# Kernel tuning notes

Measured on AMD Instinct MI355X. Metric: run time of the kernel, lower is better.

Reference implementation:

```python
import jax, jax.numpy as jnp
import numpy as np
from jax import lax

STRIDE = 2
PADDING = 2
EPS = 1e-5


def _conv1d(x, w):
    # x: (N, C_in, T), w: (C_out, C_in, K) -> (N, C_out, T_out)
    return lax.conv_general_dilated(
        x, w, window_strides=(STRIDE,), padding=[(PADDING, PADDING)],
        dimension_numbers=("NCH", "OIH", "NCH"))


def setup_inputs() -> dict:
    key = jax.random.key(0)
    ks = jax.random.split(key, 5)
    Batch, num_sensors, in_c, out_c, k, T, r = 32, 8, 64, 128, 5, 2048, 8
    x = jax.random.normal(ks[0], (Batch * num_sensors, in_c, T), dtype=jnp.float32)
    A_flat = jax.random.normal(ks[1], (Batch, r * in_c * k), dtype=jnp.float32) * 0.02
    B_flat = jax.random.normal(ks[2], (Batch, out_c * r), dtype=jnp.float32) * 0.02
    fan_in = in_c * k
    conv_w = jax.random.normal(ks[3], (out_c, in_c, k), dtype=jnp.float32) / np.sqrt(fan_in)
    conv_b = jax.random.normal(ks[4], (out_c,), dtype=jnp.float32) * 0.01
    gamma = jnp.ones((out_c,), dtype=jnp.float32)
    beta = jnp.zeros((out_c,), dtype=jnp.float32)
    return {"x": x, "A_flat": A_flat, "B_flat": B_flat,
            "conv_w": conv_w, "conv_b": conv_b, "gamma": gamma, "beta": beta,
            "num_sensors": num_sensors, "r": r, "lora_scale": 0.5}


def reference(x, A_flat, B_flat, conv_w, conv_b, gamma, beta, num_sensors, r, lora_scale):
    Batch = A_flat.shape[0]
    out_c, in_c, k = conv_w.shape
    T = x.shape[-1]

    # base conv1d
    out_base = _conv1d(x, conv_w) + conv_b[None, :, None]  # (B*S, out_c, T_out)

    # dynamic per-sample LoRA delta weight: delta_W = B @ A, (Batch, out_c, in_c, k)
    A = A_flat.reshape(Batch, r, in_c * k)
    B_mat = B_flat.reshape(Batch, out_c, r)
    delta_W = jnp.einsum("bor,brm->bom", B_mat, A).reshape(Batch, out_c, in_c, k)
    delta_W = delta_W * lora_scale

    # per-sample conv: sensors of one sample share that sample's delta weight
    x_b = x.reshape(Batch, num_sensors, in_c, T)
    lora_out = jax.vmap(_conv1d)(x_b, delta_W)  # (Batch, S, out_c, T_out)
    lora_out = lora_out.reshape(Batch * num_sensors, out_c, -1)

    out = jax.nn.relu(out_base + lora_out)

    # GroupNorm, num_groups = min(4, out_c) reduced until divisible
    G = min(4, out_c)
    while out_c % G != 0:
        G -= 1
    N, C, To = out.shape
    og = out.reshape(N, G, C // G, To)
    mean = og.mean(axis=(2, 3), keepdims=True)
    var = og.var(axis=(2, 3), keepdims=True)
    normed = ((og - mean) * lax.rsqrt(var + EPS)).reshape(N, C, To)
    return normed * gamma[None, :, None] + beta[None, :, None]
```

## Files before the change

kernel.cpp:

```cpp
#include <hip/hip_runtime.h>
#include <hip/hip_bf16.h>

#define EPSV 1e-5f
#define PITCH 36
#define TILE_SH (66 * PITCH)
#define WTILE_SH (2 * TILE_SH)

typedef short bf16x8 __attribute__((ext_vector_type(8)));
typedef short bf16x4 __attribute__((ext_vector_type(4)));
typedef float f32x4  __attribute__((ext_vector_type(4)));

__device__ __forceinline__ short f2bf(float f){
  unsigned u = __float_as_uint(f);
  u += 0x7fff + ((u >> 16) & 1);
  return (short)(u >> 16);
}
__device__ __forceinline__ int pk2(float a, float b){
  __hip_bfloat162 h = __float22bfloat162_rn(float2{a, b});
  return *reinterpret_cast<int*>(&h);
}

__global__ void build_weights(const float* __restrict__ A_flat,
                              const float* __restrict__ B_flat,
                              const float* __restrict__ conv_w,
                              const float* __restrict__ scale_p,
                              short* __restrict__ Wb){
  int idx = blockIdx.x * 256 + threadIdx.x;
  int ci = idx & 63;
  int co = (idx >> 6) & 127;
  int bj = idx >> 13;
  int b  = bj / 5;
  int j  = bj - 5 * b;
  int m  = ci * 5 + j;
  const float* Bp = B_flat + (b * 128 + co) * 8;
  const float* Ap = A_flat + b * 8 * 320 + m;
  float d = 0.f;
#pragma unroll
  for (int r = 0; r < 8; ++r) d = fmaf(Bp[r], Ap[r * 320], d);
  float w = conv_w[co * 320 + m] + scale_p[0] * d;
  Wb[idx] = f2bf(w);
}

__global__ __launch_bounds__(512, 4)
void conv_gn_mfma(const float* __restrict__ x,
                  const short* __restrict__ Wb,
                  const float* __restrict__ conv_b,
                  const float* __restrict__ gamma,
                  const float* __restrict__ beta,
                  float* __restrict__ out){
  __shared__ short xt[8 * WTILE_SH];
  __shared__ float redS[8], redQ[8], bc2[2];

  const int bid    = blockIdx.x;
  const int sample = ((bid & 7) << 5) + (bid >> 5);
  const int g      = (bid >> 3) & 3;
  const int b      = sample >> 3;
  const int tid    = threadIdx.x;
  const int lane   = tid & 63;
  const int wid    = tid >> 6;
  const int l16    = lane & 15;
  const int lk     = lane >> 4;

  short* xe = xt + wid * WTILE_SH;
  short* xo = xe + TILE_SH;

  f32x4 acc[2][8];
#pragma unroll
  for (int m2 = 0; m2 < 2; ++m2)
#pragma unroll
    for (int n = 0; n < 8; ++n) acc[m2][n] = (f32x4){0.f,0.f,0.f,0.f};

  const size_t wb_base = (size_t)b * 5 * 128 * 64;
  const float* xsamp = x + (size_t)sample * 64 * 2048;

#pragma unroll
  for (int ph = 0; ph < 4; ++ph) {
    const int ch = ph >> 1;
    const int th = ph & 1;
    const int T0 = th * 512 + wid * 64;

    const float* xb = xsamp + (size_t)(ch * 32) * 2048;

    {
      const int c = 2 * T0 + 2 * (int)lane;
#pragma unroll
      for (int rg = 0; rg < 8; ++rg) {
        const float* r = xb + (size_t)(rg * 4) * 2048 + c;
        float2 v0 = *(const float2*)(r);
        float2 v1 = *(const float2*)(r + 2048);
        float2 v2 = *(const float2*)(r + 4096);
        float2 v3 = *(const float2*)(r + 6144);
        int2 ev = { pk2(v0.x, v1.x), pk2(v2.x, v3.x) };
        int2 od = { pk2(v0.y, v1.y), pk2(v2.y, v3.y) };
        *(int2*)(xe + (lane + 1) * PITCH + rg * 4) = ev;
        *(int2*)(xo + (lane + 1) * PITCH + rg * 4) = od;
      }
      if (lane < 32) {
        const int ci = lane;
        float2 h{0.f, 0.f};
        if (T0 > 0) h = *(const float2*)(xb + (size_t)ci * 2048 + (2 * T0 - 2));
        xe[ci] = f2bf(h.x);
        xo[ci] = f2bf(h.y);
      } else {
        const int ci = lane - 32;
        const int xc = 2 * T0 + 128;
        float v = (xc < 2048) ? xb[(size_t)ci * 2048 + xc] : 0.f;
        xe[65 * PITCH + ci] = f2bf(v);
      }
    }

#pragma unroll
    for (int j = 0; j < 5; ++j) {
      const short* apb = Wb + wb_base + (size_t)(j * 128 + g * 32) * 64 + ch * 32 + lk * 8;
      bf16x8 a0 = *(const bf16x8*)(apb + (size_t)l16 * 64);
      bf16x8 a1 = *(const bf16x8*)(apb + (size_t)(l16 + 16) * 64);
      const short* arr = (j & 1) ? xo : xe;
      const int joff = (j & 1) ? ((j - 1) >> 1) : (j >> 1);
#pragma unroll
      for (int nn = 0; nn < 4; ++nn) {
        int tl = nn * 16 + l16;
        const short* bp = arr + (tl + joff) * PITCH + lk * 8;
        bf16x4 lo = *(const bf16x4*)bp;
        bf16x4 hi = *(const bf16x4*)(bp + 4);
        bf16x8 bfr = {lo[0],lo[1],lo[2],lo[3],hi[0],hi[1],hi[2],hi[3]};
        const int n = th * 4 + nn;
        acc[0][n] = __builtin_amdgcn_mfma_f32_16x16x32_bf16(a0, bfr, acc[0][n], 0, 0, 0);
        acc[1][n] = __builtin_amdgcn_mfma_f32_16x16x32_bf16(a1, bfr, acc[1][n], 0, 0, 0);
      }
    }
  }

  float cb_[2][4], ga_[2][4], be_[2][4];
#pragma unroll
  for (int m2 = 0; m2 < 2; ++m2)
#pragma unroll
    for (int r = 0; r < 4; ++r) {
      int co = g * 32 + m2 * 16 + lk * 4 + r;
      cb_[m2][r] = conv_b[co];
      ga_[m2][r] = gamma[co];
      be_[m2][r] = beta[co];
    }
  float s1 = 0.f, s2 = 0.f;
#pragma unroll
  for (int m2 = 0; m2 < 2; ++m2)
#pragma unroll
    for (int n = 0; n < 8; ++n)
#pragma unroll
      for (int r = 0; r < 4; ++r) {
        float v = acc[m2][n][r] + cb_[m2][r];
        v = v > 0.f ? v : 0.f;
        acc[m2][n][r] = v;
        s1 += v;
        s2 = fmaf(v, v, s2);
      }
#pragma unroll
  for (int off = 32; off; off >>= 1) {
    s1 += __shfl_down(s1, off);
    s2 += __shfl_down(s2, off);
  }
  if (lane == 0) { redS[wid] = s1; redQ[wid] = s2; }
  __syncthreads();
  if (tid == 0) {
    float a = 0.f, q = 0.f;
#pragma unroll
    for (int w = 0; w < 8; ++w) { a += redS[w]; q += redQ[w]; }
    float mean = a * (1.f / 32768.f);
    float var  = q * (1.f / 32768.f) - mean * mean;
    bc2[0] = mean;
    bc2[1] = rsqrtf(var + EPSV);
  }
  __syncthreads();
  const float mean = bc2[0], inv = bc2[1];
  float* ob = out + (size_t)sample * 128 * 1024;
#pragma unroll
  for (int m2 = 0; m2 < 2; ++m2)
#pragma unroll
    for (int r = 0; r < 4; ++r) {
      int co = g * 32 + m2 * 16 + lk * 4 + r;
      float aa = ga_[m2][r] * inv;
      float bb = be_[m2][r] - mean * aa;
      float* orow = ob + (size_t)co * 1024 + l16;
#pragma unroll
      for (int n = 0; n < 8; ++n) {
        int t = (n >> 2) * 512 + wid * 64 + (n & 3) * 16;
        orow[t] = acc[m2][n][r] * aa + bb;
      }
    }
}

extern "C" void kernel_launch(void* const* d_in, const int* in_sizes, int n_in,
                              void* d_out, int out_size, void* d_ws, size_t ws_size,
                              hipStream_t stream) {
  const float* x       = (const float*)d_in[0];
  const float* A_flat  = (const float*)d_in[1];
  const float* B_flat  = (const float*)d_in[2];
  const float* conv_w  = (const float*)d_in[3];
  const float* conv_b  = (const float*)d_in[4];
  const float* gamma   = (const float*)d_in[5];
  const float* beta    = (const float*)d_in[6];
  const float* scale_p = (const float*)d_in[9];

  float* out = (float*)d_out;
  short* Wb  = (short*)d_ws;

  build_weights<<<5120, 256, 0, stream>>>(A_flat, B_flat, conv_w, scale_p, Wb);
  conv_gn_mfma<<<1024, 512, 0, stream>>>(x, Wb, conv_b, gamma, beta, out);
}
```

Measured before the change: 111.5 us.

## Pre-transpose input to bf16 time-major layout and read MMA operands directly

Adds a separate transpose kernel that converts x to a padded bf16 (time, channel) layout in the workspace, so the conv kernel loads MFMA B fragments straight from global memory without per-block LDS staging. Each conv block previously rebuilt the converted tile four times (once per output-channel group), and this pass removes that repeated fp32 load and convert work. In exchange it adds a full extra read and write of a bf16 copy of x plus one more launch. It falls back to the old kernel when the workspace is too small.

```diff
diff --git a/kernel.cpp b/kernel.cpp
--- a/kernel.cpp
+++ b/kernel.cpp
@@ -2,9 +2,6 @@
 #include <hip/hip_bf16.h>
 
 #define EPSV 1e-5f
-#define PITCH 36
-#define TILE_SH (66 * PITCH)
-#define WTILE_SH (2 * TILE_SH)
 
 typedef short bf16x8 __attribute__((ext_vector_type(8)));
 typedef short bf16x4 __attribute__((ext_vector_type(4)));
@@ -41,14 +38,64 @@
   Wb[idx] = f2bf(w);
 }
 
+#define XP 66
+__global__ __launch_bounds__(256, 8)
+void xpose(const float* __restrict__ x, short* __restrict__ xT){
+  __shared__ short xl[512 * XP];
+  const int bid  = blockIdx.x;
+  const int s    = bid >> 2;
+  const int q    = bid & 3;
+  const int tid  = threadIdx.x;
+  const int lane = tid & 63;
+  const int wid  = tid >> 6;
+
+  const float* xs = x + (size_t)s * 64 * 2048 + q * 512;
+#pragma unroll
+  for (int grp = 0; grp < 4; ++grp) {
+    const int ci0 = wid * 16 + grp * 4;
+    const float* xr = xs + (size_t)ci0 * 2048;
+#pragma unroll
+    for (int pass = 0; pass < 2; ++pass) {
+      int c0 = pass * 256 + lane * 4;
+      float4 v0 = *(const float4*)(xr + c0);
+      float4 v1 = *(const float4*)(xr + c0 + 2048);
+      float4 v2 = *(const float4*)(xr + c0 + 4096);
+      float4 v3 = *(const float4*)(xr + c0 + 6144);
+      const float a0[4] = {v0.x, v0.y, v0.z, v0.w};
+      const float a1[4] = {v1.x, v1.y, v1.z, v1.w};
+      const float a2[4] = {v2.x, v2.y, v2.z, v2.w};
+      const float a3[4] = {v3.x, v3.y, v3.z, v3.w};
+#pragma unroll
+      for (int k = 0; k < 4; ++k) {
+        int base = (c0 + k) * XP + ci0;
+        *(int*)&xl[base]     = pk2(a0[k], a1[k]);
+        *(int*)&xl[base + 2] = pk2(a2[k], a3[k]);
+      }
+    }
+  }
+  __syncthreads();
+
+  short* dst = xT + ((size_t)s * 2052 + 2 + q * 512) * 64;
+  const int ci4 = lane & 15;
+#pragma unroll
+  for (int it = 0; it < 32; ++it) {
+    int col = wid * 128 + it * 4 + (lane >> 4);
+    int base = col * XP + ci4 * 4;
+    int r0 = *(const int*)&xl[base];
+    int r1 = *(const int*)&xl[base + 2];
+    *(int2*)(dst + (size_t)col * 64 + ci4 * 4) = int2{r0, r1};
+  }
+  if (q == 0 && tid < 64) ((int*)(xT + (size_t)s * 2052 * 64))[tid] = 0;
+  if (q == 3 && tid < 64) ((int*)(xT + ((size_t)s * 2052 + 2050) * 64))[tid] = 0;
+}
+
 __global__ __launch_bounds__(512, 4)
-void conv_gn_mfma(const float* __restrict__ x,
-                  const short* __restrict__ Wb,
-                  const float* __restrict__ conv_b,
-                  const float* __restrict__ gamma,
-                  const float* __restrict__ beta,
-                  float* __restrict__ out){
-  __shared__ short xt[8 * WTILE_SH];
+void conv_gn_direct(const short* __restrict__ xT,
+                    const short* __restrict__ Wb,
+                    const float* __restrict__ conv_b,
+                    const float* __restrict__ gamma,
+                    const float* __restrict__ beta,
+                    float* __restrict__ out){
   __shared__ float redS[8], redQ[8], bc2[2];
 
   const int bid    = blockIdx.x;
@@ -60,55 +107,148 @@
   const int wid    = tid >> 6;
   const int l16    = lane & 15;
   const int lk     = lane >> 4;
-
+  const int T0     = wid << 7;
+
+  f32x4 acc[2][8];
+#pragma unroll
+  for (int m2 = 0; m2 < 2; ++m2)
+#pragma unroll
+    for (int n = 0; n < 8; ++n) acc[m2][n] = (f32x4){0.f,0.f,0.f,0.f};
+
+  const size_t wb_base = (size_t)b * 5 * 128 * 64;
+
+#pragma unroll
+  for (int ch = 0; ch < 2; ++ch) {
+    const short* xbase = xT + ((size_t)sample * 2052 + 2 * (T0 + l16)) * 64
+                            + ch * 32 + lk * 8;
+#pragma unroll
+    for (int j = 0; j < 5; ++j) {
+      const short* apb = Wb + wb_base + (size_t)(j * 128 + g * 32) * 64 + ch * 32 + lk * 8;
+      bf16x8 a0 = *(const bf16x8*)(apb + (size_t)l16 * 64);
+      bf16x8 a1 = *(const bf16x8*)(apb + (size_t)(l16 + 16) * 64);
+#pragma unroll
+      for (int nn = 0; nn < 8; ++nn) {
+        bf16x8 bfr = *(const bf16x8*)(xbase + nn * 2048 + j * 64);
+        acc[0][nn] = __builtin_amdgcn_mfma_f32_16x16x32_bf16(a0, bfr, acc[0][nn], 0, 0, 0);
+        acc[1][nn] = __builtin_amdgcn_mfma_f32_16x16x32_bf16(a1, bfr, acc[1][nn], 0, 0, 0);
+      }
+    }
+  }
+
+  float cb_[2][4], ga_[2][4], be_[2][4];
+#pragma unroll
+  for (int m2 = 0; m2 < 2; ++m2)
+#pragma unroll
+    for (int r = 0; r < 4; ++r) {
+      int co = g * 32 + m2 * 16 + lk * 4 + r;
+      cb_[m2][r] = conv_b[co];
+      ga_[m2][r] = gamma[co];
+      be_[m2][r] = beta[co];
+    }
+  float s1 = 0.f, s2 = 0.f;
+#pragma unroll
+  for (int m2 = 0; m2 < 2; ++m2)
+#pragma unroll
+    for (int n = 0; n < 8; ++n)
+#pragma unroll
+      for (int r = 0; r < 4; ++r) {
+        float v = acc[m2][n][r] + cb_[m2][r];
+        v = v > 0.f ? v : 0.f;
+        acc[m2][n][r] = v;
+        s1 += v;
+        s2 = fmaf(v, v, s2);
+      }
+#pragma unroll
+  for (int off = 32; off; off >>= 1) {
+    s1 += __shfl_down(s1, off);
+    s2 += __shfl_down(s2, off);
+  }
+  if (lane == 0) { redS[wid] = s1; redQ[wid] = s2; }
+  __syncthreads();
+  if (tid == 0) {
+    float a = 0.f, q = 0.f;
+#pragma unroll
+    for (int w = 0; w < 8; ++w) { a += redS[w]; q += redQ[w]; }
+    float mean = a * (1.f / 32768.f);
+    float var  = q * (1.f / 32768.f) - mean * mean;
+    bc2[0] = mean;
+    bc2[1] = rsqrtf(var + EPSV);
+  }
+  __syncthreads();
+  const float mean = bc2[0], inv = bc2[1];
+  float* ob = out + (size_t)sample * 128 * 1024;
+#pragma unroll
+  for (int m2 = 0; m2 < 2; ++m2)
+#pragma unroll
+    for (int r = 0; r < 4; ++r) {
+      int co = g * 32 + m2 * 16 + lk * 4 + r;
+      float aa = ga_[m2][r] * inv;
+      float bb = be_[m2][r] - mean * aa;
+      float* orow = ob + (size_t)co * 1024 + T0 + l16;
+#pragma unroll
+      for (int n = 0; n < 8; ++n)
+        orow[n * 16] = acc[m2][n][r] * aa + bb;
+    }
+}
+
+#define PITCH 36
+#define TILE_SH (66 * PITCH)
+#define WTILE_SH (2 * TILE_SH)
+__global__ __launch_bounds__(512, 4)
+void conv_gn_fallback(const float* __restrict__ x,
+                      const short* __restrict__ Wb,
+                      const float* __restrict__ conv_b,
+                      const float* __restrict__ gamma,
+                      const float* __restrict__ beta,
+                      float* __restrict__ out){
+  __shared__ short xt[8 * WTILE_SH];
+  __shared__ float redS[8], redQ[8], bc2[2];
+  const int bid    = blockIdx.x;
+  const int sample = ((bid & 7) << 5) + (bid >> 5);
+  const int g      = (bid >> 3) & 3;
+  const int b      = sample >> 3;
+  const int tid    = threadIdx.x;
+  const int lane   = tid & 63;
+  const int wid    = tid >> 6;
+  const int l16    = lane & 15;
+  const int lk     = lane >> 4;
   short* xe = xt + wid * WTILE_SH;
   short* xo = xe + TILE_SH;
-
   f32x4 acc[2][8];
 #pragma unroll
   for (int m2 = 0; m2 < 2; ++m2)
 #pragma unroll
     for (int n = 0; n < 8; ++n) acc[m2][n] = (f32x4){0.f,0.f,0.f,0.f};
-
   const size_t wb_base = (size_t)b * 5 * 128 * 64;
   const float* xsamp = x + (size_t)sample * 64 * 2048;
-
 #pragma unroll
   for (int ph = 0; ph < 4; ++ph) {
-    const int ch = ph >> 1;
-    const int th = ph & 1;
+    const int ch = ph >> 1, th = ph & 1;
     const int T0 = th * 512 + wid * 64;
-
     const float* xb = xsamp + (size_t)(ch * 32) * 2048;
-
-    {
-      const int c = 2 * T0 + 2 * (int)lane;
-#pragma unroll
-      for (int rg = 0; rg < 8; ++rg) {
-        const float* r = xb + (size_t)(rg * 4) * 2048 + c;
-        float2 v0 = *(const float2*)(r);
-        float2 v1 = *(const float2*)(r + 2048);
-        float2 v2 = *(const float2*)(r + 4096);
-        float2 v3 = *(const float2*)(r + 6144);
-        int2 ev = { pk2(v0.x, v1.x), pk2(v2.x, v3.x) };
-        int2 od = { pk2(v0.y, v1.y), pk2(v2.y, v3.y) };
-        *(int2*)(xe + (lane + 1) * PITCH + rg * 4) = ev;
-        *(int2*)(xo + (lane + 1) * PITCH + rg * 4) = od;
-      }
-      if (lane < 32) {
-        const int ci = lane;
-        float2 h{0.f, 0.f};
-        if (T0 > 0) h = *(const float2*)(xb + (size_t)ci * 2048 + (2 * T0 - 2));
-        xe[ci] = f2bf(h.x);
-        xo[ci] = f2bf(h.y);
-      } else {
-        const int ci = lane - 32;
-        const int xc = 2 * T0 + 128;
-        float v = (xc < 2048) ? xb[(size_t)ci * 2048 + xc] : 0.f;
-        xe[65 * PITCH + ci] = f2bf(v);
-      }
-    }
-
+    const int c = 2 * T0 + 2 * (int)lane;
+#pragma unroll
+    for (int rg = 0; rg < 8; ++rg) {
+      const float* r = xb + (size_t)(rg * 4) * 2048 + c;
+      float2 v0 = *(const float2*)(r);
+      float2 v1 = *(const float2*)(r + 2048);
+      float2 v2 = *(const float2*)(r + 4096);
+      float2 v3 = *(const float2*)(r + 6144);
+      int2 ev = { pk2(v0.x, v1.x), pk2(v2.x, v3.x) };
+      int2 od = { pk2(v0.y, v1.y), pk2(v2.y, v3.y) };
+      *(int2*)(xe + (lane + 1) * PITCH + rg * 4) = ev;
+      *(int2*)(xo + (lane + 1) * PITCH + rg * 4) = od;
+    }
+    if (lane < 32) {
+      float2 h{0.f, 0.f};
+      if (T0 > 0) h = *(const float2*)(xb + (size_t)lane * 2048 + (2 * T0 - 2));
+      xe[lane] = f2bf(h.x);
+      xo[lane] = f2bf(h.y);
+    } else {
+      const int ci = lane - 32, xc = 2 * T0 + 128;
+      float v = (xc < 2048) ? xb[(size_t)ci * 2048 + xc] : 0.f;
+      xe[65 * PITCH + ci] = f2bf(v);
+    }
 #pragma unroll
     for (int j = 0; j < 5; ++j) {
       const short* apb = Wb + wb_base + (size_t)(j * 128 + g * 32) * 64 + ch * 32 + lk * 8;
@@ -129,16 +269,13 @@
       }
     }
   }
-
   float cb_[2][4], ga_[2][4], be_[2][4];
 #pragma unroll
   for (int m2 = 0; m2 < 2; ++m2)
 #pragma unroll
     for (int r = 0; r < 4; ++r) {
       int co = g * 32 + m2 * 16 + lk * 4 + r;
-      cb_[m2][r] = conv_b[co];
-      ga_[m2][r] = gamma[co];
-      be_[m2][r] = beta[co];
+      cb_[m2][r] = conv_b[co]; ga_[m2][r] = gamma[co]; be_[m2][r] = beta[co];
     }
   float s1 = 0.f, s2 = 0.f;
 #pragma unroll
@@ -149,15 +286,10 @@
       for (int r = 0; r < 4; ++r) {
         float v = acc[m2][n][r] + cb_[m2][r];
         v = v > 0.f ? v : 0.f;
-        acc[m2][n][r] = v;
-        s1 += v;
-        s2 = fmaf(v, v, s2);
-      }
-#pragma unroll
-  for (int off = 32; off; off >>= 1) {
-    s1 += __shfl_down(s1, off);
-    s2 += __shfl_down(s2, off);
-  }
+        acc[m2][n][r] = v; s1 += v; s2 = fmaf(v, v, s2);
+      }
+#pragma unroll
+  for (int off = 32; off; off >>= 1) { s1 += __shfl_down(s1, off); s2 += __shfl_down(s2, off); }
   if (lane == 0) { redS[wid] = s1; redQ[wid] = s2; }
   __syncthreads();
   if (tid == 0) {
@@ -166,8 +298,7 @@
     for (int w = 0; w < 8; ++w) { a += redS[w]; q += redQ[w]; }
     float mean = a * (1.f / 32768.f);
     float var  = q * (1.f / 32768.f) - mean * mean;
-    bc2[0] = mean;
-    bc2[1] = rsqrtf(var + EPSV);
+    bc2[0] = mean; bc2[1] = rsqrtf(var + EPSV);
   }
   __syncthreads();
   const float mean = bc2[0], inv = bc2[1];
@@ -202,7 +333,14 @@
 
   float* out = (float*)d_out;
   short* Wb  = (short*)d_ws;
+  short* xT  = Wb + 32 * 5 * 128 * 64;
+  const size_t need = 2621440ull + 67239936ull;
 
   build_weights<<<5120, 256, 0, stream>>>(A_flat, B_flat, conv_w, scale_p, Wb);
-  conv_gn_mfma<<<1024, 512, 0, stream>>>(x, Wb, conv_b, gamma, beta, out);
-}
+  if (ws_size >= need) {
+    xpose<<<1024, 256, 0, stream>>>(x, xT);
+    conv_gn_direct<<<1024, 512, 0, stream>>>(xT, Wb, conv_b, gamma, beta, out);
+  } else {
+    conv_gn_fallback<<<1024, 512, 0, stream>>>(x, Wb, conv_b, gamma, beta, out);
+  }
+}
```

New measurement: 165.1 us. 1.48x slower.
